# Kernel tuning notes

Measured on AMD Instinct MI355X. Metric: run time of the kernel, lower is better.

## Reference

```python
import jax, jax.numpy as jnp
import numpy as np

NUM_HEADS = 8
HEAD_DIM = 64
HIDDEN = 512
ROPE_THETA = 500000.0


def _make_rope(seq_len, head_dim, theta):
    inv_freq = 1.0 / (theta ** (np.arange(0, head_dim, 2, dtype=np.float32) / head_dim))
    t = np.arange(seq_len, dtype=np.float32)
    freqs = np.outer(t, inv_freq)                  # [S, hd/2]
    emb = np.concatenate([freqs, freqs], axis=-1)  # [S, hd]
    return jnp.asarray(np.cos(emb)), jnp.asarray(np.sin(emb))


def setup_inputs() -> dict:
    key = jax.random.key(0)
    ks = jax.random.split(key, 5)
    B, S, H = 1, 4096, HIDDEN
    num_registers = 32
    hidden_states = jax.random.normal(ks[0], (B, S, H), dtype=jnp.float32)
    scale = 0.02
    Wq = jax.random.normal(ks[1], (H, H), dtype=jnp.float32) * scale
    Wk = jax.random.normal(ks[2], (H, H), dtype=jnp.float32) * scale
    Wv = jax.random.normal(ks[3], (H, H), dtype=jnp.float32) * scale
    Wo = jax.random.normal(ks[4], (H, H), dtype=jnp.float32) * scale
    cos, sin = _make_rope(S - num_registers, HEAD_DIM, ROPE_THETA)
    return {"hidden_states": hidden_states, "Wq": Wq, "Wk": Wk, "Wv": Wv,
            "Wo": Wo, "cos": cos, "sin": sin, "num_registers": num_registers}


def _rotate_half(x):
    x1, x2 = jnp.split(x, 2, axis=-1)
    return jnp.concatenate([-x2, x1], axis=-1)


def _apply_rope(q, k, cos, sin):
    # cos/sin: [S_real, hd] broadcast over [B, H, S_real, hd]
    cos = cos[None, None]
    sin = sin[None, None]
    return q * cos + _rotate_half(q) * sin, k * cos + _rotate_half(k) * sin


def reference(hidden_states, Wq, Wk, Wv, Wo, cos, sin, num_registers):
    B, S, _ = hidden_states.shape
    def proj(W):
        # torch Linear: x @ W.T -> [B, S, H] -> [B, nh, S, hd]
        y = jnp.einsum('bsh,oh->bso', hidden_states, W)
        return y.reshape(B, S, NUM_HEADS, HEAD_DIM).transpose(0, 2, 1, 3)
    q, k, v = proj(Wq), proj(Wk), proj(Wv)

    if num_registers > 0:
        q_reg, q_real = q[:, :, :num_registers], q[:, :, num_registers:]
        k_reg, k_real = k[:, :, :num_registers], k[:, :, num_registers:]
        q_real, k_real = _apply_rope(q_real, k_real, cos, sin)
        q = jnp.concatenate([q_reg, q_real], axis=2)
        k = jnp.concatenate([k_reg, k_real], axis=2)
    else:
        q, k = _apply_rope(q, k, cos, sin)

    scale = 1.0 / jnp.sqrt(jnp.float32(HEAD_DIM))
    scores = jnp.einsum('bhqd,bhkd->bhqk', q, k) * scale  # [B, nh, S, S]
    causal = jnp.tril(jnp.ones((S, S), dtype=bool))
    scores = jnp.where(causal[None, None], scores, jnp.float32(-1e30))
    attn = jax.nn.softmax(scores, axis=-1)
    out = jnp.einsum('bhqk,bhkd->bhqd', attn, v)
    out = out.transpose(0, 2, 1, 3).reshape(B, S, HIDDEN)
    return jnp.einsum('bsh,oh->bso', out, Wo)
```

## Files before the change

kernel.cpp:

```cpp
#include <hip/hip_runtime.h>
#include <cstdint>
#include <cstddef>

#define S_LEN 4096
#define HID   512
#define NHEAD 8
#define HD    64
#define SCALE_LOG2E 0.1803368801111204f

typedef __bf16 bf16;
typedef __bf16 bf16x8 __attribute__((ext_vector_type(8)));
typedef __bf16 bf16x4 __attribute__((ext_vector_type(4)));
typedef float  f32x4  __attribute__((ext_vector_type(4)));

__device__ __forceinline__ bf16x8 cvt8(float4 a, float4 b) {
    bf16x8 o;
    o[0] = (bf16)a.x; o[1] = (bf16)a.y; o[2] = (bf16)a.z; o[3] = (bf16)a.w;
    o[4] = (bf16)b.x; o[5] = (bf16)b.y; o[6] = (bf16)b.z; o[7] = (bf16)b.w;
    return o;
}

__global__ __launch_bounds__(256) void gemm_qkv(
    const float* __restrict__ Xf,
    const float* __restrict__ W0, const float* __restrict__ W1, const float* __restrict__ W2,
    const float* __restrict__ cosT, const float* __restrict__ sinT,
    const int* __restrict__ nregp,
    bf16* __restrict__ Qh, bf16* __restrict__ Kh, bf16* __restrict__ Vt)
{
    const int z = blockIdx.z;
    const float* W = (z == 0) ? W0 : (z == 1 ? W1 : W2);
    const int m0 = blockIdx.y * 64, n0 = blockIdx.x * 128;
    __shared__ bf16 lA[64][8][8];
    __shared__ bf16 lB[128][8][8];
    const int tid = threadIdx.x;
    const int lane = tid & 63, w = tid >> 6;
    const int l16 = lane & 15, lc = lane >> 4, l7 = lane & 7;
    const int wm = (w & 1) * 32, wn = (w >> 1) * 64;
    f32x4 acc[2][4] = {};

    for (int k0 = 0; k0 < HID; k0 += 64) {
        __syncthreads();
#pragma unroll
        for (int i = 0; i < 2; i++) {
            int uu = tid + 256 * i;
            int m = uu >> 3, c = uu & 7;
            const float* p = Xf + (size_t)(m0 + m) * HID + k0 + 8 * c;
            *(bf16x8*)(&lA[m][c ^ (m & 7)][0]) =
                cvt8(*(const float4*)p, *(const float4*)(p + 4));
        }
#pragma unroll
        for (int i = 0; i < 4; i++) {
            int uu = tid + 256 * i;
            int m = uu >> 3, c = uu & 7;
            const float* p = W + (size_t)(n0 + m) * HID + k0 + 8 * c;
            *(bf16x8*)(&lB[m][c ^ (m & 7)][0]) =
                cvt8(*(const float4*)p, *(const float4*)(p + 4));
        }
        __syncthreads();
#pragma unroll
        for (int ks = 0; ks < 2; ks++) {
            bf16x8 af[2], bfr[4];
#pragma unroll
            for (int i = 0; i < 2; i++)
                af[i]  = *(const bf16x8*)(&lA[wm + 16 * i + l16][(4 * ks + lc) ^ l7][0]);
#pragma unroll
            for (int j = 0; j < 4; j++)
                bfr[j] = *(const bf16x8*)(&lB[wn + 16 * j + l16][(4 * ks + lc) ^ l7][0]);
#pragma unroll
            for (int i = 0; i < 2; i++)
#pragma unroll
                for (int j = 0; j < 4; j++)
                    acc[i][j] = __builtin_amdgcn_mfma_f32_16x16x32_bf16(
                        af[i], bfr[j], acc[i][j], 0, 0, 0);
        }
    }

    const int h = (n0 + wn) >> 6;
    if (z == 2) {
#pragma unroll
        for (int i = 0; i < 2; i++) {
            const int s0r = m0 + wm + 16 * i + 4 * lc;
#pragma unroll
            for (int j = 0; j < 4; j++) {
                const int dl = 16 * j + l16;
                bf16x4 o;
#pragma unroll
                for (int r = 0; r < 4; r++) o[r] = (bf16)acc[i][j][r];
                *(bf16x4*)(Vt + ((size_t)(h * HD + dl)) * S_LEN + s0r) = o;
            }
        }
    } else {
        const int nreg = *nregp;
        bf16* dst = (z == 0) ? Qh : Kh;
#pragma unroll
        for (int i = 0; i < 2; i++) {
            const int s0r = m0 + wm + 16 * i + 4 * lc;
#pragma unroll
            for (int r = 0; r < 4; r++) {
                const int s = s0r + r;
                float c0 = 1.f, sn0 = 0.f, c1 = 1.f, sn1 = 0.f;
                if (s >= nreg) {
                    const int p = s - nreg;
                    c0  = cosT[(size_t)p * HD + l16];
                    sn0 = sinT[(size_t)p * HD + l16];
                    c1  = cosT[(size_t)p * HD + 16 + l16];
                    sn1 = sinT[(size_t)p * HD + 16 + l16];
                }
                const float x0 = acc[i][0][r], x1 = acc[i][1][r];
                const float x2 = acc[i][2][r], x3 = acc[i][3][r];
                bf16* row = dst + ((size_t)h * S_LEN + s) * HD;
                row[l16]      = (bf16)(x0 * c0 - x2 * sn0);
                row[l16 + 16] = (bf16)(x1 * c1 - x3 * sn1);
                row[l16 + 32] = (bf16)(x2 * c0 + x0 * sn0);
                row[l16 + 48] = (bf16)(x3 * c1 + x1 * sn1);
            }
        }
    }
}

__global__ __launch_bounds__(256) void gemm_out(
    const bf16* __restrict__ X, const float* __restrict__ Wf,
    float* __restrict__ Y)
{
    const int m0 = blockIdx.y * 64, n0 = blockIdx.x * 64;
    __shared__ bf16 lA[64][8][8];
    __shared__ bf16 lB[64][8][8];
    const int tid = threadIdx.x;
    const int lane = tid & 63, w = tid >> 6;
    const int l16 = lane & 15, lc = lane >> 4, l7 = lane & 7;
    const int wm = (w & 1) * 32, wn = (w >> 1) * 32;
    f32x4 acc[2][2] = {};

    for (int k0 = 0; k0 < HID; k0 += 64) {
        __syncthreads();
#pragma unroll
        for (int i = 0; i < 2; i++) {
            int uu = tid + 256 * i;
            int m = uu >> 3, c = uu & 7;
            *(bf16x8*)(&lA[m][c ^ (m & 7)][0]) =
                *(const bf16x8*)(X + (size_t)(m0 + m) * HID + k0 + 8 * c);
        }
#pragma unroll
        for (int i = 0; i < 2; i++) {
            int uu = tid + 256 * i;
            int m = uu >> 3, c = uu & 7;
            const float* p = Wf + (size_t)(n0 + m) * HID + k0 + 8 * c;
            *(bf16x8*)(&lB[m][c ^ (m & 7)][0]) =
                cvt8(*(const float4*)p, *(const float4*)(p + 4));
        }
        __syncthreads();
#pragma unroll
        for (int ks = 0; ks < 2; ks++) {
            bf16x8 af[2], bfr[2];
#pragma unroll
            for (int i = 0; i < 2; i++) {
                af[i]  = *(const bf16x8*)(&lA[wm + 16 * i + l16][(4 * ks + lc) ^ l7][0]);
                bfr[i] = *(const bf16x8*)(&lB[wn + 16 * i + l16][(4 * ks + lc) ^ l7][0]);
            }
#pragma unroll
            for (int i = 0; i < 2; i++)
#pragma unroll
                for (int j = 0; j < 2; j++)
                    acc[i][j] = __builtin_amdgcn_mfma_f32_16x16x32_bf16(
                        af[i], bfr[j], acc[i][j], 0, 0, 0);
        }
    }
#pragma unroll
    for (int i = 0; i < 2; i++) {
        int row = m0 + wm + 16 * i + 4 * lc;
#pragma unroll
        for (int j = 0; j < 2; j++) {
            int col = n0 + wn + 16 * j + l16;
#pragma unroll
            for (int r = 0; r < 4; r++)
                Y[(size_t)(row + r) * HID + col] = acc[i][j][r];
        }
    }
}

__global__ __launch_bounds__(256) void attn_part(
    const bf16* __restrict__ Qh, const bf16* __restrict__ Kh,
    const bf16* __restrict__ Vt, float* __restrict__ Opart,
    float* __restrict__ Lpart)
{
    const int h = blockIdx.x >> 2;
    const int ch = blockIdx.x & 3;
    const int bt = 63 - (int)blockIdx.y;
    const int qb = bt * 64;
    const int nkt = bt + 1;
    const int k0 = (nkt * ch) >> 2;
    const int k1 = (nkt * (ch + 1)) >> 2;
    const int tid = threadIdx.x;
    const int lane = tid & 63, w = tid >> 6;
    const int l16 = lane & 15, lc = lane >> 4, l7 = lane & 7;

    float* Op = Opart + ((size_t)(h * 64 + bt) * 4 + ch) * 4096;
    float* Lp = Lpart + ((size_t)(h * 64 + bt) * 4 + ch) * 64;

    if (k0 >= k1) {
        const f32x4 z = {0.f, 0.f, 0.f, 0.f};
#pragma unroll
        for (int i = 0; i < 4; i++)
            *(f32x4*)(Op + 4 * (tid + 256 * i)) = z;
        if (tid < 64) Lp[tid] = 0.f;
        return;
    }

    __shared__ bf16 lK[2][64][8][8];
    __shared__ bf16 lV[2][64][8][8];
    __shared__ bf16 lPT[4][16][76];

    const bf16* Kb_ = Kh + (size_t)h * S_LEN * HD;
    const bf16* Vb_ = Vt + (size_t)h * HD * S_LEN;

    int srow[2], scol[2];
#pragma unroll
    for (int i = 0; i < 2; i++) {
        int uu = tid + 256 * i;
        srow[i] = uu >> 3;
        scol[i] = uu & 7;
    }

    bf16x8 qf[2];
    {
        const bf16* qrow = Qh + (size_t)h * S_LEN * HD + (size_t)(qb + 16 * w + l16) * HD;
        qf[0] = *(const bf16x8*)(qrow + 8 * lc);
        qf[1] = *(const bf16x8*)(qrow + 32 + 8 * lc);
    }
    f32x4 oacc[4] = {};
    float l_sum = 0.f;

    {
        bf16x8 kr[2], vr[2];
#pragma unroll
        for (int i = 0; i < 2; i++) {
            kr[i] = *(const bf16x8*)(Kb_ + (size_t)(k0 * 64 + srow[i]) * HD + 8 * scol[i]);
            vr[i] = *(const bf16x8*)(Vb_ + (size_t)srow[i] * S_LEN + k0 * 64 + 8 * scol[i]);
        }
#pragma unroll
        for (int i = 0; i < 2; i++) {
            *(bf16x8*)(&lK[0][srow[i]][scol[i] ^ (srow[i] & 7)][0]) = kr[i];
            *(bf16x8*)(&lV[0][srow[i]][scol[i] ^ (srow[i] & 7)][0]) = vr[i];
        }
    }

    int cur = 0;
    for (int kt = k0; kt < k1; kt++) {
        __syncthreads();

        bf16x8 kr[2], vr[2];
        if (kt + 1 < k1) {
#pragma unroll
            for (int i = 0; i < 2; i++) {
                kr[i] = *(const bf16x8*)(Kb_ + (size_t)((kt + 1) * 64 + srow[i]) * HD +
                                         8 * scol[i]);
                vr[i] = *(const bf16x8*)(Vb_ + (size_t)srow[i] * S_LEN +
                                         (kt + 1) * 64 + 8 * scol[i]);
            }
        }

        f32x4 sacc[4] = {};
#pragma unroll
        for (int ks = 0; ks < 2; ks++)
#pragma unroll
            for (int j = 0; j < 4; j++) {
                bf16x8 kf = *(const bf16x8*)(&lK[cur][16 * j + l16][(4 * ks + lc) ^ l7][0]);
                sacc[j] = __builtin_amdgcn_mfma_f32_16x16x32_bf16(
                    kf, qf[ks], sacc[j], 0, 0, 0);
            }

        float pv[4][4];
#pragma unroll
        for (int j = 0; j < 4; j++)
#pragma unroll
            for (int r = 0; r < 4; r++)
                pv[j][r] = __builtin_amdgcn_exp2f(sacc[j][r] * SCALE_LOG2E);
        if (kt == nkt - 1) {
            const int qg = qb + 16 * w + l16;
#pragma unroll
            for (int j = 0; j < 4; j++)
#pragma unroll
                for (int r = 0; r < 4; r++) {
                    const int keyg = kt * 64 + 16 * j + 4 * lc + r;
                    if (keyg > qg) pv[j][r] = 0.f;
                }
        }
#pragma unroll
        for (int j = 0; j < 4; j++)
            l_sum += (pv[j][0] + pv[j][1]) + (pv[j][2] + pv[j][3]);

#pragma unroll
        for (int j = 0; j < 4; j++) {
            bf16x4 pp;
#pragma unroll
            for (int r = 0; r < 4; r++) pp[r] = (bf16)pv[j][r];
            *(bf16x4*)(&lPT[w][l16][16 * j + 4 * lc]) = pp;
        }
        bf16x8 pb[2];
#pragma unroll
        for (int ks = 0; ks < 2; ks++)
            pb[ks] = *(const bf16x8*)(&lPT[w][l16][32 * ks + 8 * lc]);

#pragma unroll
        for (int ks = 0; ks < 2; ks++)
#pragma unroll
            for (int j = 0; j < 4; j++) {
                bf16x8 vf = *(const bf16x8*)(&lV[cur][16 * j + l16][(4 * ks + lc) ^ l7][0]);
                oacc[j] = __builtin_amdgcn_mfma_f32_16x16x32_bf16(
                    vf, pb[ks], oacc[j], 0, 0, 0);
            }

        if (kt + 1 < k1) {
#pragma unroll
            for (int i = 0; i < 2; i++) {
                *(bf16x8*)(&lK[cur ^ 1][srow[i]][scol[i] ^ (srow[i] & 7)][0]) = kr[i];
                *(bf16x8*)(&lV[cur ^ 1][srow[i]][scol[i] ^ (srow[i] & 7)][0]) = vr[i];
            }
        }
        cur ^= 1;
    }

    l_sum += __shfl_xor(l_sum, 16, 64);
    l_sum += __shfl_xor(l_sum, 32, 64);
    if (lane < 16) Lp[16 * w + l16] = l_sum;

#pragma unroll
    for (int j = 0; j < 4; j++)
        *(f32x4*)(Op + (size_t)(16 * w + l16) * 64 + 16 * j + 4 * lc) = oacc[j];
}

__global__ __launch_bounds__(256) void attn_combine(
    const float* __restrict__ Opart, const float* __restrict__ Lpart,
    bf16* __restrict__ Ob)
{
    const int h = blockIdx.x, bt = blockIdx.y;
    const size_t base = (size_t)(h * 64 + bt) * 4;
    const float* O0 = Opart + base * 4096;
    const float* L0 = Lpart + base * 64;
    const int t = threadIdx.x;
    const int q = t >> 2, dq = (t & 3) * 16;
    const float l = (L0[q] + L0[64 + q]) + (L0[128 + q] + L0[192 + q]);
    const float inv = 1.0f / l;
    bf16* out = Ob + (size_t)(bt * 64 + q) * HID + h * HD + dq;
#pragma unroll
    for (int g = 0; g < 2; g++) {
        bf16x8 o8;
#pragma unroll
        for (int e = 0; e < 2; e++) {
            const int off = q * 64 + dq + 8 * g + 4 * e;
            f32x4 a = *(const f32x4*)(O0 + off);
            f32x4 b = *(const f32x4*)(O0 + 4096 + off);
            f32x4 c = *(const f32x4*)(O0 + 8192 + off);
            f32x4 d = *(const f32x4*)(O0 + 12288 + off);
#pragma unroll
            for (int r = 0; r < 4; r++)
                o8[4 * e + r] = (bf16)(((a[r] + b[r]) + (c[r] + d[r])) * inv);
        }
        *(bf16x8*)(out + 8 * g) = o8;
    }
}

extern "C" void kernel_launch(void* const* d_in, const int* in_sizes, int n_in,
                              void* d_out, int out_size, void* d_ws, size_t ws_size,
                              hipStream_t stream) {
    const float* hs   = (const float*)d_in[0];
    const float* Wq   = (const float*)d_in[1];
    const float* Wk   = (const float*)d_in[2];
    const float* Wv   = (const float*)d_in[3];
    const float* Wo   = (const float*)d_in[4];
    const float* cosT = (const float*)d_in[5];
    const float* sinT = (const float*)d_in[6];
    const int*   nreg = (const int*)d_in[7];

    char* ws = (char*)d_ws;
    const size_t MiB = 1 << 20;
    bf16*  Qh    = (bf16*)(ws);
    bf16*  Kh    = (bf16*)(ws + 4 * MiB);
    bf16*  Vt    = (bf16*)(ws + 8 * MiB);
    bf16*  Ob    = (bf16*)(ws + 12 * MiB);
    float* Opart = (float*)(ws + 16 * MiB);
    float* Lpart = (float*)(ws + 48 * MiB);

    gemm_qkv<<<dim3(4, 64, 3), 256, 0, stream>>>(hs, Wq, Wk, Wv,
                                                 cosT, sinT, nreg, Qh, Kh, Vt);
    attn_part<<<dim3(32, 64), 256, 0, stream>>>(Qh, Kh, Vt, Opart, Lpart);
    attn_combine<<<dim3(8, 64), 256, 0, stream>>>(Opart, Lpart, Ob);
    gemm_out<<<dim3(8, 64), 256, 0, stream>>>(Ob, Wo, (float*)d_out);
}
```

Before: 150.5 us.

## Process 128 query rows per attention block to reuse K/V tiles

Each attention workgroup now handles two 64-row query groups against every staged K/V tile, doubling MFMA work per LDS tile load and halving the grid. The partial output/sum layout and the combine kernel are updated for 128-row blocks, and a min-blocks launch bound is added. This trades more registers and some wasted masked work near the diagonal for less redundant K/V traffic.

```diff
diff --git a/kernel.cpp b/kernel.cpp
--- a/kernel.cpp
+++ b/kernel.cpp
@@ -178,37 +178,36 @@
     }
 }
 
-__global__ __launch_bounds__(256) void attn_part(
+__global__ __launch_bounds__(256, 3) void attn_part(
     const bf16* __restrict__ Qh, const bf16* __restrict__ Kh,
     const bf16* __restrict__ Vt, float* __restrict__ Opart,
     float* __restrict__ Lpart)
 {
     const int h = blockIdx.x >> 2;
     const int ch = blockIdx.x & 3;
-    const int bt = 63 - (int)blockIdx.y;
-    const int qb = bt * 64;
-    const int nkt = bt + 1;
+    const int qb = 31 - (int)blockIdx.y;
+    const int nkt = 2 * qb + 2;
     const int k0 = (nkt * ch) >> 2;
     const int k1 = (nkt * (ch + 1)) >> 2;
     const int tid = threadIdx.x;
     const int lane = tid & 63, w = tid >> 6;
     const int l16 = lane & 15, lc = lane >> 4, l7 = lane & 7;
 
-    float* Op = Opart + ((size_t)(h * 64 + bt) * 4 + ch) * 4096;
-    float* Lp = Lpart + ((size_t)(h * 64 + bt) * 4 + ch) * 64;
+    float* Op = Opart + ((size_t)((h * 32 + qb) * 4 + ch)) * 8192;
+    float* Lp = Lpart + ((size_t)((h * 32 + qb) * 4 + ch)) * 128;
 
     if (k0 >= k1) {
         const f32x4 z = {0.f, 0.f, 0.f, 0.f};
 #pragma unroll
-        for (int i = 0; i < 4; i++)
+        for (int i = 0; i < 8; i++)
             *(f32x4*)(Op + 4 * (tid + 256 * i)) = z;
-        if (tid < 64) Lp[tid] = 0.f;
+        if (tid < 128) Lp[tid] = 0.f;
         return;
     }
 
     __shared__ bf16 lK[2][64][8][8];
     __shared__ bf16 lV[2][64][8][8];
-    __shared__ bf16 lPT[4][16][76];
+    __shared__ bf16 lPT[4][2][16][76];
 
     const bf16* Kb_ = Kh + (size_t)h * S_LEN * HD;
     const bf16* Vb_ = Vt + (size_t)h * HD * S_LEN;
@@ -221,14 +220,16 @@
         scol[i] = uu & 7;
     }
 
-    bf16x8 qf[2];
-    {
-        const bf16* qrow = Qh + (size_t)h * S_LEN * HD + (size_t)(qb + 16 * w + l16) * HD;
-        qf[0] = *(const bf16x8*)(qrow + 8 * lc);
-        qf[1] = *(const bf16x8*)(qrow + 32 + 8 * lc);
-    }
-    f32x4 oacc[4] = {};
-    float l_sum = 0.f;
+    bf16x8 qf[2][2];
+#pragma unroll
+    for (int g = 0; g < 2; g++) {
+        const bf16* qrow = Qh + (size_t)h * S_LEN * HD +
+                           (size_t)(qb * 128 + g * 64 + 16 * w + l16) * HD;
+        qf[g][0] = *(const bf16x8*)(qrow + 8 * lc);
+        qf[g][1] = *(const bf16x8*)(qrow + 32 + 8 * lc);
+    }
+    f32x4 oacc[2][4] = {};
+    float l_sum[2] = {0.f, 0.f};
 
     {
         bf16x8 kr[2], vr[2];
@@ -259,55 +260,63 @@
             }
         }
 
-        f32x4 sacc[4] = {};
+        f32x4 s0[4] = {}, s1[4] = {};
 #pragma unroll
         for (int ks = 0; ks < 2; ks++)
 #pragma unroll
             for (int j = 0; j < 4; j++) {
                 bf16x8 kf = *(const bf16x8*)(&lK[cur][16 * j + l16][(4 * ks + lc) ^ l7][0]);
-                sacc[j] = __builtin_amdgcn_mfma_f32_16x16x32_bf16(
-                    kf, qf[ks], sacc[j], 0, 0, 0);
-            }
-
-        float pv[4][4];
-#pragma unroll
-        for (int j = 0; j < 4; j++)
-#pragma unroll
-            for (int r = 0; r < 4; r++)
-                pv[j][r] = __builtin_amdgcn_exp2f(sacc[j][r] * SCALE_LOG2E);
-        if (kt == nkt - 1) {
-            const int qg = qb + 16 * w + l16;
+                s0[j] = __builtin_amdgcn_mfma_f32_16x16x32_bf16(kf, qf[0][ks], s0[j], 0, 0, 0);
+                s1[j] = __builtin_amdgcn_mfma_f32_16x16x32_bf16(kf, qf[1][ks], s1[j], 0, 0, 0);
+            }
+
+        const bool near_diag = (kt >= nkt - 2);
+#pragma unroll
+        for (int g = 0; g < 2; g++) {
+            const f32x4* sg = g ? s1 : s0;
+            float pv[4][4];
 #pragma unroll
             for (int j = 0; j < 4; j++)
 #pragma unroll
-                for (int r = 0; r < 4; r++) {
-                    const int keyg = kt * 64 + 16 * j + 4 * lc + r;
-                    if (keyg > qg) pv[j][r] = 0.f;
-                }
-        }
-#pragma unroll
-        for (int j = 0; j < 4; j++)
-            l_sum += (pv[j][0] + pv[j][1]) + (pv[j][2] + pv[j][3]);
-
-#pragma unroll
-        for (int j = 0; j < 4; j++) {
-            bf16x4 pp;
-#pragma unroll
-            for (int r = 0; r < 4; r++) pp[r] = (bf16)pv[j][r];
-            *(bf16x4*)(&lPT[w][l16][16 * j + 4 * lc]) = pp;
-        }
-        bf16x8 pb[2];
-#pragma unroll
-        for (int ks = 0; ks < 2; ks++)
-            pb[ks] = *(const bf16x8*)(&lPT[w][l16][32 * ks + 8 * lc]);
-
+                for (int r = 0; r < 4; r++)
+                    pv[j][r] = __builtin_amdgcn_exp2f(sg[j][r] * SCALE_LOG2E);
+            if (near_diag) {
+                const int qg = qb * 128 + g * 64 + 16 * w + l16;
+#pragma unroll
+                for (int j = 0; j < 4; j++)
+#pragma unroll
+                    for (int r = 0; r < 4; r++) {
+                        const int keyg = kt * 64 + 16 * j + 4 * lc + r;
+                        if (keyg > qg) pv[j][r] = 0.f;
+                    }
+            }
+#pragma unroll
+            for (int j = 0; j < 4; j++)
+                l_sum[g] += (pv[j][0] + pv[j][1]) + (pv[j][2] + pv[j][3]);
+#pragma unroll
+            for (int j = 0; j < 4; j++) {
+                bf16x4 pp;
+#pragma unroll
+                for (int r = 0; r < 4; r++) pp[r] = (bf16)pv[j][r];
+                *(bf16x4*)(&lPT[w][g][l16][16 * j + 4 * lc]) = pp;
+            }
+        }
+
+        bf16x8 pb[2][2];
+#pragma unroll
+        for (int g = 0; g < 2; g++)
+#pragma unroll
+            for (int ks = 0; ks < 2; ks++)
+                pb[g][ks] = *(const bf16x8*)(&lPT[w][g][l16][32 * ks + 8 * lc]);
 #pragma unroll
         for (int ks = 0; ks < 2; ks++)
 #pragma unroll
             for (int j = 0; j < 4; j++) {
                 bf16x8 vf = *(const bf16x8*)(&lV[cur][16 * j + l16][(4 * ks + lc) ^ l7][0]);
-                oacc[j] = __builtin_amdgcn_mfma_f32_16x16x32_bf16(
-                    vf, pb[ks], oacc[j], 0, 0, 0);
+                oacc[0][j] = __builtin_amdgcn_mfma_f32_16x16x32_bf16(
+                    vf, pb[0][ks], oacc[0][j], 0, 0, 0);
+                oacc[1][j] = __builtin_amdgcn_mfma_f32_16x16x32_bf16(
+                    vf, pb[1][ks], oacc[1][j], 0, 0, 0);
             }
 
         if (kt + 1 < k1) {
@@ -320,38 +329,42 @@
         cur ^= 1;
     }
 
-    l_sum += __shfl_xor(l_sum, 16, 64);
-    l_sum += __shfl_xor(l_sum, 32, 64);
-    if (lane < 16) Lp[16 * w + l16] = l_sum;
-
-#pragma unroll
-    for (int j = 0; j < 4; j++)
-        *(f32x4*)(Op + (size_t)(16 * w + l16) * 64 + 16 * j + 4 * lc) = oacc[j];
+#pragma unroll
+    for (int g = 0; g < 2; g++) {
+        float ls = l_sum[g];
+        ls += __shfl_xor(ls, 16, 64);
+        ls += __shfl_xor(ls, 32, 64);
+        if (lane < 16) Lp[g * 64 + 16 * w + l16] = ls;
+#pragma unroll
+        for (int j = 0; j < 4; j++)
+            *(f32x4*)(Op + (size_t)(g * 64 + 16 * w + l16) * 64 + 16 * j + 4 * lc) =
+                oacc[g][j];
+    }
 }
 
 __global__ __launch_bounds__(256) void attn_combine(
     const float* __restrict__ Opart, const float* __restrict__ Lpart,
     bf16* __restrict__ Ob)
 {
-    const int h = blockIdx.x, bt = blockIdx.y;
-    const size_t base = (size_t)(h * 64 + bt) * 4;
-    const float* O0 = Opart + base * 4096;
-    const float* L0 = Lpart + base * 64;
+    const int h = blockIdx.x, qb = blockIdx.y;
+    const size_t base = (size_t)((h * 32 + qb) * 4);
+    const float* O0 = Opart + base * 8192;
+    const float* L0 = Lpart + base * 128;
     const int t = threadIdx.x;
-    const int q = t >> 2, dq = (t & 3) * 16;
-    const float l = (L0[q] + L0[64 + q]) + (L0[128 + q] + L0[192 + q]);
+    const int q = t >> 1, dh = (t & 1) * 32;
+    const float l = (L0[q] + L0[128 + q]) + (L0[256 + q] + L0[384 + q]);
     const float inv = 1.0f / l;
-    bf16* out = Ob + (size_t)(bt * 64 + q) * HID + h * HD + dq;
-#pragma unroll
-    for (int g = 0; g < 2; g++) {
+    bf16* out = Ob + (size_t)(qb * 128 + q) * HID + h * HD + dh;
+#pragma unroll
+    for (int g = 0; g < 4; g++) {
+        const int off = q * 64 + dh + 8 * g;
         bf16x8 o8;
 #pragma unroll
         for (int e = 0; e < 2; e++) {
-            const int off = q * 64 + dq + 8 * g + 4 * e;
-            f32x4 a = *(const f32x4*)(O0 + off);
-            f32x4 b = *(const f32x4*)(O0 + 4096 + off);
-            f32x4 c = *(const f32x4*)(O0 + 8192 + off);
-            f32x4 d = *(const f32x4*)(O0 + 12288 + off);
+            f32x4 a = *(const f32x4*)(O0 + off + 4 * e);
+            f32x4 b = *(const f32x4*)(O0 + 8192 + off + 4 * e);
+            f32x4 c = *(const f32x4*)(O0 + 16384 + off + 4 * e);
+            f32x4 d = *(const f32x4*)(O0 + 24576 + off + 4 * e);
 #pragma unroll
             for (int r = 0; r < 4; r++)
                 o8[4 * e + r] = (bf16)(((a[r] + b[r]) + (c[r] + d[r])) * inv);
@@ -379,11 +392,11 @@
     bf16*  Vt    = (bf16*)(ws + 8 * MiB);
     bf16*  Ob    = (bf16*)(ws + 12 * MiB);
     float* Opart = (float*)(ws + 16 * MiB);
-    float* Lpart = (float*)(ws + 48 * MiB);
+    float* Lpart = (float*)(ws + 50 * MiB);
 
     gemm_qkv<<<dim3(4, 64, 3), 256, 0, stream>>>(hs, Wq, Wk, Wv,
                                                  cosT, sinT, nreg, Qh, Kh, Vt);
-    attn_part<<<dim3(32, 64), 256, 0, stream>>>(Qh, Kh, Vt, Opart, Lpart);
-    attn_combine<<<dim3(8, 64), 256, 0, stream>>>(Opart, Lpart, Ob);
+    attn_part<<<dim3(32, 32), 256, 0, stream>>>(Qh, Kh, Vt, Opart, Lpart);
+    attn_combine<<<dim3(8, 32), 256, 0, stream>>>(Opart, Lpart, Ob);
     gemm_out<<<dim3(8, 64), 256, 0, stream>>>(Ob, Wo, (float*)d_out);
 }
```

Result: no change. 152.3 us (+1.2%).

## Pre-convert inputs and weights to bf16 and stage Q/K stores through LDS

Applied to the files above, without the earlier changes.

Adds a conversion kernel that casts the hidden states and all four weight matrices to bf16 once, so the GEMM kernels load bf16 directly instead of reloading and converting fp32 tiles in every block. The QKV kernel also writes the rotary-embedded Q/K tile into a shared-memory scratch buffer and then stores full coalesced 16-byte rows to global memory, replacing scattered 2-byte stores. The cost is an extra kernel launch plus a full fp32 read and bf16 write of the inputs, and more LDS per block.

```diff
diff --git a/kernel.cpp b/kernel.cpp
--- a/kernel.cpp
+++ b/kernel.cpp
@@ -13,25 +13,42 @@
 typedef __bf16 bf16x4 __attribute__((ext_vector_type(4)));
 typedef float  f32x4  __attribute__((ext_vector_type(4)));
 
-__device__ __forceinline__ bf16x8 cvt8(float4 a, float4 b) {
-    bf16x8 o;
-    o[0] = (bf16)a.x; o[1] = (bf16)a.y; o[2] = (bf16)a.z; o[3] = (bf16)a.w;
-    o[4] = (bf16)b.x; o[5] = (bf16)b.y; o[6] = (bf16)b.z; o[7] = (bf16)b.w;
-    return o;
+__global__ __launch_bounds__(256) void cvt_in(
+    const float* __restrict__ hs, const float* __restrict__ wq,
+    const float* __restrict__ wk, const float* __restrict__ wv,
+    const float* __restrict__ wo,
+    bf16* __restrict__ xb, bf16* __restrict__ wqb, bf16* __restrict__ wkb,
+    bf16* __restrict__ wvb, bf16* __restrict__ wob)
+{
+    int e = (blockIdx.x * 256 + threadIdx.x) * 4;
+    const float* s; bf16* d; int o;
+    if (e < 2 * 1024 * 1024) { s = hs; d = xb; o = e; }
+    else {
+        int t = e - 2 * 1024 * 1024;
+        int wi = t >> 18;
+        o = t & ((1 << 18) - 1);
+        s = (wi == 0) ? wq : (wi == 1) ? wk : (wi == 2) ? wv : wo;
+        d = (wi == 0) ? wqb : (wi == 1) ? wkb : (wi == 2) ? wvb : wob;
+    }
+    const float4 v = *(const float4*)(s + o);
+    bf16x4 ob;
+    ob[0] = (bf16)v.x; ob[1] = (bf16)v.y; ob[2] = (bf16)v.z; ob[3] = (bf16)v.w;
+    *(bf16x4*)(d + o) = ob;
 }
 
 __global__ __launch_bounds__(256) void gemm_qkv(
-    const float* __restrict__ Xf,
-    const float* __restrict__ W0, const float* __restrict__ W1, const float* __restrict__ W2,
+    const bf16* __restrict__ Xb,
+    const bf16* __restrict__ W0, const bf16* __restrict__ W1, const bf16* __restrict__ W2,
     const float* __restrict__ cosT, const float* __restrict__ sinT,
     const int* __restrict__ nregp,
     bf16* __restrict__ Qh, bf16* __restrict__ Kh, bf16* __restrict__ Vt)
 {
     const int z = blockIdx.z;
-    const float* W = (z == 0) ? W0 : (z == 1 ? W1 : W2);
+    const bf16* W = (z == 0) ? W0 : (z == 1 ? W1 : W2);
     const int m0 = blockIdx.y * 64, n0 = blockIdx.x * 128;
     __shared__ bf16 lA[64][8][8];
     __shared__ bf16 lB[128][8][8];
+    __shared__ bf16 scratch[64][136];
     const int tid = threadIdx.x;
     const int lane = tid & 63, w = tid >> 6;
     const int l16 = lane & 15, lc = lane >> 4, l7 = lane & 7;
@@ -44,17 +61,15 @@
         for (int i = 0; i < 2; i++) {
             int uu = tid + 256 * i;
             int m = uu >> 3, c = uu & 7;
-            const float* p = Xf + (size_t)(m0 + m) * HID + k0 + 8 * c;
             *(bf16x8*)(&lA[m][c ^ (m & 7)][0]) =
-                cvt8(*(const float4*)p, *(const float4*)(p + 4));
+                *(const bf16x8*)(Xb + (size_t)(m0 + m) * HID + k0 + 8 * c);
         }
 #pragma unroll
         for (int i = 0; i < 4; i++) {
             int uu = tid + 256 * i;
             int m = uu >> 3, c = uu & 7;
-            const float* p = W + (size_t)(n0 + m) * HID + k0 + 8 * c;
             *(bf16x8*)(&lB[m][c ^ (m & 7)][0]) =
-                cvt8(*(const float4*)p, *(const float4*)(p + 4));
+                *(const bf16x8*)(W + (size_t)(n0 + m) * HID + k0 + 8 * c);
         }
         __syncthreads();
 #pragma unroll
@@ -75,8 +90,8 @@
         }
     }
 
-    const int h = (n0 + wn) >> 6;
     if (z == 2) {
+        const int h = (n0 + wn) >> 6;
 #pragma unroll
         for (int i = 0; i < 2; i++) {
             const int s0r = m0 + wm + 16 * i + 4 * lc;
@@ -94,10 +109,10 @@
         bf16* dst = (z == 0) ? Qh : Kh;
 #pragma unroll
         for (int i = 0; i < 2; i++) {
-            const int s0r = m0 + wm + 16 * i + 4 * lc;
+            const int sl0 = wm + 16 * i + 4 * lc;
 #pragma unroll
             for (int r = 0; r < 4; r++) {
-                const int s = s0r + r;
+                const int s = m0 + sl0 + r;
                 float c0 = 1.f, sn0 = 0.f, c1 = 1.f, sn1 = 0.f;
                 if (s >= nreg) {
                     const int p = s - nreg;
@@ -108,18 +123,28 @@
                 }
                 const float x0 = acc[i][0][r], x1 = acc[i][1][r];
                 const float x2 = acc[i][2][r], x3 = acc[i][3][r];
-                bf16* row = dst + ((size_t)h * S_LEN + s) * HD;
+                bf16* row = &scratch[sl0 + r][wn];
                 row[l16]      = (bf16)(x0 * c0 - x2 * sn0);
                 row[l16 + 16] = (bf16)(x1 * c1 - x3 * sn1);
                 row[l16 + 32] = (bf16)(x2 * c0 + x0 * sn0);
                 row[l16 + 48] = (bf16)(x3 * c1 + x1 * sn1);
             }
         }
+        __syncthreads();
+        const int h0 = n0 >> 6;
+#pragma unroll
+        for (int i = 0; i < 4; i++) {
+            int u = tid + 256 * i;
+            int row = u >> 4, c = u & 15;
+            bf16x8 val = *(const bf16x8*)(&scratch[row][c * 8]);
+            *(bf16x8*)(dst + ((size_t)(h0 + (c >> 3)) * S_LEN + m0 + row) * HD +
+                       (c & 7) * 8) = val;
+        }
     }
 }
 
 __global__ __launch_bounds__(256) void gemm_out(
-    const bf16* __restrict__ X, const float* __restrict__ Wf,
+    const bf16* __restrict__ X, const bf16* __restrict__ Wb,
     float* __restrict__ Y)
 {
     const int m0 = blockIdx.y * 64, n0 = blockIdx.x * 64;
@@ -144,9 +169,8 @@
         for (int i = 0; i < 2; i++) {
             int uu = tid + 256 * i;
             int m = uu >> 3, c = uu & 7;
-            const float* p = Wf + (size_t)(n0 + m) * HID + k0 + 8 * c;
             *(bf16x8*)(&lB[m][c ^ (m & 7)][0]) =
-                cvt8(*(const float4*)p, *(const float4*)(p + 4));
+                *(const bf16x8*)(Wb + (size_t)(n0 + m) * HID + k0 + 8 * c);
         }
         __syncthreads();
 #pragma unroll
@@ -380,10 +404,16 @@
     bf16*  Ob    = (bf16*)(ws + 12 * MiB);
     float* Opart = (float*)(ws + 16 * MiB);
     float* Lpart = (float*)(ws + 48 * MiB);
-
-    gemm_qkv<<<dim3(4, 64, 3), 256, 0, stream>>>(hs, Wq, Wk, Wv,
+    bf16*  Xb    = (bf16*)(ws + 49 * MiB);
+    bf16*  Wqb   = (bf16*)(ws + 53 * MiB);
+    bf16*  Wkb   = (bf16*)(ws + 53 * MiB + 512 * 1024);
+    bf16*  Wvb   = (bf16*)(ws + 54 * MiB);
+    bf16*  Wob   = (bf16*)(ws + 54 * MiB + 512 * 1024);
+
+    cvt_in<<<3072, 256, 0, stream>>>(hs, Wq, Wk, Wv, Wo, Xb, Wqb, Wkb, Wvb, Wob);
+    gemm_qkv<<<dim3(4, 64, 3), 256, 0, stream>>>(Xb, Wqb, Wkb, Wvb,
                                                  cosT, sinT, nreg, Qh, Kh, Vt);
     attn_part<<<dim3(32, 64), 256, 0, stream>>>(Qh, Kh, Vt, Opart, Lpart);
     attn_combine<<<dim3(8, 64), 256, 0, stream>>>(Opart, Lpart, Ob);
-    gemm_out<<<dim3(8, 64), 256, 0, stream>>>(Ob, Wo, (float*)d_out);
-}
+    gemm_out<<<dim3(8, 64), 256, 0, stream>>>(Ob, Wob, (float*)d_out);
+}
```

Result: faster. 142.5 us (-5.3%).
